# Optimization experiments

Hardware: AMD Instinct MI355X
Metric: run time of the kernel (lower is better)

The kernel has to match this reference:

```python
import jax, jax.numpy as jnp
import numpy as np

N, K = 150000, 27
C1, C2 = 64, 64
CLAMP = 1.0


def _lrelu(v):
    return jnp.where(v >= 0, v, 0.2 * v)


def _sparse_conv(feats, nbr_idx, W):
    # feats: [N, Cin], nbr_idx: [N, K], W: [K, Cin, Cout]
    # gather-GEMM-scatter sparse conv; scan over the 27 fixed kernel offsets
    acc0 = jnp.zeros((feats.shape[0], W.shape[-1]), feats.dtype)

    def step(acc, kw):
        idx, Wk = kw  # idx: [N], Wk: [Cin, Cout]
        return acc + feats[idx] @ Wk, None

    acc, _ = jax.lax.scan(step, acc0, (nbr_idx.T, W))
    return acc


def _bottleneck(x, nbr_idx, w1, w2, w3):
    h = _lrelu(_sparse_conv(x, nbr_idx, w1))  # kxkxk conv
    h = _lrelu(h @ w2)                        # 1x1x1 conv
    return _sparse_conv(h, nbr_idx, w3)       # kxkxk conv


def setup_inputs() -> dict:
    key = jax.random.key(0)
    ks = jax.random.split(key, 14)
    x = jax.random.normal(ks[0], (N, C1 + C2), jnp.float32)
    nbr_idx = jax.random.randint(ks[1], (N, K), 0, N, jnp.int32)
    s = 0.1  # xavier-like small scale
    d = {"x": x, "nbr_idx": nbr_idx}
    names = ["g1", "g2", "h1", "h2"]
    for i, nm in enumerate(names):
        d[nm + "_w1"] = jax.random.normal(ks[2 + 3 * i], (K, C2 if nm in ("g2", "h2") else C1, C1 if nm in ("g2", "h2") else C2), jnp.float32) * s
        co = C1 if nm in ("g2", "h2") else C2
        d[nm + "_w2"] = jax.random.normal(ks[3 + 3 * i], (co, co), jnp.float32) * s
        d[nm + "_w3"] = jax.random.normal(ks[4 + 3 * i], (K, co, co), jnp.float32) * s
    return d


def reference(x, nbr_idx, g1_w1, g1_w2, g1_w3, g2_w1, g2_w2, g2_w3,
              h1_w1, h1_w2, h1_w3, h2_w1, h2_w2, h2_w3):
    x1 = x[:, :C1]
    x2 = x[:, C1:C1 + C2]
    # forward (reverse=False) affine coupling
    s1 = jnp.exp(CLAMP * (jax.nn.sigmoid(_bottleneck(x2, nbr_idx, g2_w1, g2_w2, g2_w3)) * 2 - 1))
    y1 = x1 * s1 + _bottleneck(x2, nbr_idx, h2_w1, h2_w2, h2_w3)
    s2 = jnp.exp(CLAMP * (jax.nn.sigmoid(_bottleneck(y1, nbr_idx, g1_w1, g1_w2, g1_w3)) * 2 - 1))
    y2 = x2 * s2 + _bottleneck(y1, nbr_idx, h1_w1, h1_w2, h1_w3)
    return jnp.concatenate([y1, y2], axis=1)
```

## Files before the change

### kernel.cpp

```cpp
#include <hip/hip_runtime.h>
#include <stdint.h>

typedef unsigned short u16;
typedef __bf16 bf16x8 __attribute__((ext_vector_type(8)));
typedef float f32x4 __attribute__((ext_vector_type(4)));

#define NNODES 150000
#define KNBR 27
#define LDX 128
#define MR 64
#define APAD 72
#define WSU 8192

#define WAITVM(N) asm volatile("s_waitcnt vmcnt(" #N ")" ::: "memory")

static __device__ __forceinline__ void gl_lds16(const u16* g, u16* l){
  __builtin_amdgcn_global_load_lds((const __attribute__((address_space(1))) void*)g,
                                   (__attribute__((address_space(3))) void*)l, 16, 0, 0);
}

static __device__ __forceinline__ u16 f2bf(float f){
  union { float f; uint32_t i; } v; v.f = f;
  uint32_t x = v.i;
  uint32_t r = (x + 0x7fffu + ((x >> 16) & 1u)) >> 16;
  return (u16)r;
}
static __device__ __forceinline__ float lrelu(float v){ return v >= 0.f ? v : 0.2f*v; }

__global__ void reformat_w(const float* __restrict__ src, u16* __restrict__ dst, int ksteps){
  int idx = blockIdx.x*256 + threadIdx.x;
  int total = ksteps*4*64;
  if (idx >= total) return;
  int lane = idx & 63;
  int ctile = (idx >> 6) & 3;
  int t = idx >> 8;
  int quad = lane >> 4, m = lane & 15;
  union { u16 h[8]; float4 v; } tmp;
  const float* s = src + ((size_t)(t*32 + quad*8))*64 + ctile*16 + m;
  #pragma unroll
  for (int j=0;j<8;j++) tmp.h[j] = f2bf(s[j*64]);
  *reinterpret_cast<float4*>(dst + (size_t)idx*8) = tmp.v;
}

__global__ void conv_x2(const float* __restrict__ x, u16* __restrict__ sb){
  int idx = blockIdx.x*256 + threadIdx.x;
  int e = idx*8;
  if (e >= NNODES*64) return;
  int row = e >> 6, col = e & 63;
  const float* s = x + (size_t)row*LDX + 64 + col;
  float4 a = *reinterpret_cast<const float4*>(s);
  float4 b = *reinterpret_cast<const float4*>(s+4);
  union { u16 h[8]; float4 v; } t;
  t.h[0]=f2bf(a.x); t.h[1]=f2bf(a.y); t.h[2]=f2bf(a.z); t.h[3]=f2bf(a.w);
  t.h[4]=f2bf(b.x); t.h[5]=f2bf(b.y); t.h[6]=f2bf(b.z); t.h[7]=f2bf(b.w);
  *reinterpret_cast<float4*>(sb + e) = t.v;
}

__global__ __launch_bounds__(256,4) void conv1_fused(
    const u16* __restrict__ sb,
    const int* __restrict__ nbr,
    const u16* __restrict__ wb1g, const u16* __restrict__ wb1h,
    const u16* __restrict__ wb2g, const u16* __restrict__ wb2h,
    u16* __restrict__ u)
{
  extern __shared__ char smem[];
  u16* ws    = (u16*)smem;
  int* s_idx = (int*)(smem + 2*WSU*2);
  u16* sa    = (u16*)smem;

  int tid = threadIdx.x;
  int row0 = blockIdx.x * MR;
  for (int i = tid; i < MR*KNBR; i += 256){
    int r = i / KNBR, kk = i - r*KNBR;
    int row = row0 + r;
    s_idx[i] = (row < NNODES) ? nbr[row*KNBR + kk] : 0;
  }
  __syncthreads();

  int lane = tid & 63;
  int wv = tid >> 6;
  int quad = lane >> 4, m = lane & 15;
  int qoff = quad * 8;
  int tt_w = wv >> 1, mat_w = wv & 1;
  const u16* wsrc = mat_w ? wb1h : wb1g;
  const int* idx = &s_idx[(wv*16 + m)*KNBR];

  f32x4 acc[2][4];
  f32x4 zz = {0.f,0.f,0.f,0.f};
  #pragma unroll
  for (int mt2=0;mt2<2;mt2++)
    #pragma unroll
    for (int i=0;i<4;i++) acc[mt2][i] = zz;

  bf16x8 as[3][2];

  #define STAGE_W1(s) { \
    u16* dst_ = ws + ((s)&1)*WSU + (tt_w*2+mat_w)*2048; \
    const u16* src_ = wsrc + ((size_t)(2*(s)+tt_w))*2048 + (size_t)lane*8; \
    _Pragma("unroll") \
    for (int ct_=0; ct_<4; ct_++) gl_lds16(src_ + ct_*512, dst_ + ct_*512); }

  #define LOAD_A1(s, d0, d1) { \
    const u16* r_ = sb + (size_t)idx[s]*64 + qoff; \
    d0 = *reinterpret_cast<const bf16x8*>(r_); \
    d1 = *reinterpret_cast<const bf16x8*>(r_ + 32); }

  STAGE_W1(0); __builtin_amdgcn_sched_barrier(0);
  LOAD_A1(0, as[0][0], as[0][1]); __builtin_amdgcn_sched_barrier(0);
  LOAD_A1(1, as[1][0], as[1][1]); __builtin_amdgcn_sched_barrier(0);
  LOAD_A1(2, as[2][0], as[2][1]);

  #pragma unroll
  for (int k=0;k<KNBR;k++){
    if (k == 0)       { WAITVM(4); }
    else if (k <= 24) { WAITVM(2); }
    else              { WAITVM(0); }
    __builtin_amdgcn_s_barrier();

    if (k+1 < KNBR) { STAGE_W1(k+1); }
    __builtin_amdgcn_sched_barrier(0);

    const u16* wsb = ws + (k&1)*WSU;
    #pragma unroll
    for (int tt=0;tt<2;tt++){
      bf16x8 af = as[k%3][tt];
      #pragma unroll
      for (int mt2=0;mt2<2;mt2++){
        #pragma unroll
        for (int ct=0;ct<4;ct++){
          bf16x8 b = *reinterpret_cast<const bf16x8*>(wsb + ((tt*2+mt2)*4+ct)*512 + (size_t)lane*8);
          acc[mt2][ct] = __builtin_amdgcn_mfma_f32_16x16x32_bf16(af, b, acc[mt2][ct], 0,0,0);
        }
      }
    }
    if (k+3 < KNBR) { LOAD_A1(k+3, as[k%3][0], as[k%3][1]); }
  }
  __syncthreads();

  #pragma unroll
  for (int mt2=0;mt2<2;mt2++){
    #pragma unroll
    for (int ct=0;ct<4;ct++){
      #pragma unroll
      for (int i=0;i<4;i++){
        int rl = wv*16 + quad*4 + i;
        sa[mt2*MR*APAD + rl*APAD + ct*16 + m] = f2bf(lrelu(acc[mt2][ct][i]));
      }
    }
  }
  f32x4 d[2][4];
  #pragma unroll
  for (int mt2=0;mt2<2;mt2++)
    #pragma unroll
    for (int i=0;i<4;i++) d[mt2][i] = zz;
  #pragma unroll
  for (int c=0;c<2;c++){
    #pragma unroll
    for (int mt2=0;mt2<2;mt2++){
      bf16x8 a = *reinterpret_cast<const bf16x8*>(&sa[mt2*MR*APAD + (wv*16 + m)*APAD + c*32 + qoff]);
      #pragma unroll
      for (int ct=0;ct<4;ct++){
        const u16* wp = (mt2 ? wb2h : wb2g) + (((size_t)c*4+ct)*64 + lane)*8;
        bf16x8 b = *reinterpret_cast<const bf16x8*>(wp);
        d[mt2][ct] = __builtin_amdgcn_mfma_f32_16x16x32_bf16(a, b, d[mt2][ct], 0,0,0);
      }
    }
  }
  #pragma unroll
  for (int mt2=0;mt2<2;mt2++){
    #pragma unroll
    for (int ct=0;ct<4;ct++){
      #pragma unroll
      for (int i=0;i<4;i++){
        int row = row0 + wv*16 + quad*4 + i;
        if (row < NNODES){
          u[(size_t)row*128 + mt2*64 + ct*16 + m] = f2bf(lrelu(d[mt2][ct][i]));
        }
      }
    }
  }
  #undef STAGE_W1
  #undef LOAD_A1
}

__global__ __launch_bounds__(256,4) void conv2_coupling(
    const u16* __restrict__ ub,
    const int* __restrict__ nbr,
    const u16* __restrict__ wbg, const u16* __restrict__ wbh,
    const float* __restrict__ x, int xcol0,
    float* __restrict__ out, int ycol0,
    u16* __restrict__ yb, int write_yb)
{
  extern __shared__ char smem[];
  u16* ws    = (u16*)smem;
  int* s_idx = (int*)(smem + 2*WSU*2);

  int tid = threadIdx.x;
  int row0 = blockIdx.x * MR;
  for (int i = tid; i < MR*KNBR; i += 256){
    int r = i / KNBR, kk = i - r*KNBR;
    int row = row0 + r;
    s_idx[i] = (row < NNODES) ? nbr[row*KNBR + kk] : 0;
  }
  __syncthreads();

  int lane = tid & 63;
  int wv = tid >> 6;
  int quad = lane >> 4, m = lane & 15;
  int qoff = quad * 8;
  int tt_w = wv >> 1, mat_w = wv & 1;
  const u16* wsrc = mat_w ? wbh : wbg;
  const int* idx = &s_idx[(wv*16 + m)*KNBR];

  f32x4 accg[4], acch[4];
  f32x4 zz = {0.f,0.f,0.f,0.f};
  #pragma unroll
  for (int i=0;i<4;i++){ accg[i]=zz; acch[i]=zz; }

  bf16x8 as[2][4];

  #define STAGE_W2(s) { \
    u16* dst_ = ws + ((s)&1)*WSU + (tt_w*2+mat_w)*2048; \
    const u16* src_ = wsrc + ((size_t)(2*(s)+tt_w))*2048 + (size_t)lane*8; \
    _Pragma("unroll") \
    for (int ct_=0; ct_<4; ct_++) gl_lds16(src_ + ct_*512, dst_ + ct_*512); }

  #define LOAD_A2(s, d0, d1, d2, d3) { \
    const u16* r_ = ub + (size_t)idx[s]*128 + qoff; \
    d0 = *reinterpret_cast<const bf16x8*>(r_); \
    d1 = *reinterpret_cast<const bf16x8*>(r_ + 32); \
    d2 = *reinterpret_cast<const bf16x8*>(r_ + 64); \
    d3 = *reinterpret_cast<const bf16x8*>(r_ + 96); }

  STAGE_W2(0); __builtin_amdgcn_sched_barrier(0);
  LOAD_A2(0, as[0][0], as[0][1], as[0][2], as[0][3]); __builtin_amdgcn_sched_barrier(0);
  LOAD_A2(1, as[1][0], as[1][1], as[1][2], as[1][3]);

  #pragma unroll
  for (int k=0;k<KNBR;k++){
    if (k <= 25) { WAITVM(4); }
    else         { WAITVM(0); }
    __builtin_amdgcn_s_barrier();

    if (k+1 < KNBR) { STAGE_W2(k+1); }
    __builtin_amdgcn_sched_barrier(0);

    const u16* wsb = ws + (k&1)*WSU;
    #pragma unroll
    for (int tt=0;tt<2;tt++){
      bf16x8 ag = as[k&1][tt];
      bf16x8 ah = as[k&1][2+tt];
      #pragma unroll
      for (int ct=0;ct<4;ct++){
        bf16x8 bg = *reinterpret_cast<const bf16x8*>(wsb + ((tt*2+0)*4+ct)*512 + (size_t)lane*8);
        accg[ct] = __builtin_amdgcn_mfma_f32_16x16x32_bf16(ag, bg, accg[ct], 0,0,0);
      }
      #pragma unroll
      for (int ct=0;ct<4;ct++){
        bf16x8 bh = *reinterpret_cast<const bf16x8*>(wsb + ((tt*2+1)*4+ct)*512 + (size_t)lane*8);
        acch[ct] = __builtin_amdgcn_mfma_f32_16x16x32_bf16(ah, bh, acch[ct], 0,0,0);
      }
    }
    if (k+2 < KNBR) { LOAD_A2(k+2, as[k&1][0], as[k&1][1], as[k&1][2], as[k&1][3]); }
  }

  #pragma unroll
  for (int ct=0;ct<4;ct++){
    #pragma unroll
    for (int i=0;i<4;i++){
      int row = row0 + wv*16 + quad*4 + i;
      if (row < NNODES){
        int col = ct*16 + m;
        float bg = accg[ct][i];
        float bh = acch[ct][i];
        float s = 1.f/(1.f + __expf(-bg));
        s = __expf(2.f*s - 1.f);
        float xv = x[(size_t)row*LDX + xcol0 + col];
        float y = xv*s + bh;
        out[(size_t)row*LDX + ycol0 + col] = y;
        if (write_yb) yb[(size_t)row*64 + col] = f2bf(y);
      }
    }
  }
  #undef STAGE_W2
  #undef LOAD_A2
}

extern "C" void kernel_launch(void* const* d_in, const int* in_sizes, int n_in,
                              void* d_out, int out_size, void* d_ws, size_t ws_size,
                              hipStream_t stream)
{
  const float* x   = (const float*)d_in[0];
  const int*   nbr = (const int*)d_in[1];
  const float* g1_w1=(const float*)d_in[2],  *g1_w2=(const float*)d_in[3],  *g1_w3=(const float*)d_in[4];
  const float* g2_w1=(const float*)d_in[5],  *g2_w2=(const float*)d_in[6],  *g2_w3=(const float*)d_in[7];
  const float* h1_w1=(const float*)d_in[8],  *h1_w2=(const float*)d_in[9],  *h1_w3=(const float*)d_in[10];
  const float* h2_w1=(const float*)d_in[11], *h2_w2=(const float*)d_in[12], *h2_w3=(const float*)d_in[13];
  float* out = (float*)d_out;
  u16* ws = (u16*)d_ws;

  const size_t WBB = (size_t)54*4*64*8;
  const size_t WBS = (size_t)2*4*64*8;
  u16* p = ws;
  u16* wb_g2_1=p; p+=WBB;  u16* wb_h2_1=p; p+=WBB;
  u16* wb_g2_2=p; p+=WBS;  u16* wb_h2_2=p; p+=WBS;
  u16* wb_g2_3=p; p+=WBB;  u16* wb_h2_3=p; p+=WBB;
  u16* wb_g1_1=p; p+=WBB;  u16* wb_h1_1=p; p+=WBB;
  u16* wb_g1_2=p; p+=WBS;  u16* wb_h1_2=p; p+=WBS;
  u16* wb_g1_3=p; p+=WBB;  u16* wb_h1_3=p; p+=WBB;
  u16* ub = p; p += (size_t)NNODES*128;
  u16* sb = p; p += (size_t)NNODES*64;

  reformat_w<<<54,256,0,stream>>>(g2_w1, wb_g2_1, 54);
  reformat_w<<<54,256,0,stream>>>(h2_w1, wb_h2_1, 54);
  reformat_w<<<2,256,0,stream>>>(g2_w2, wb_g2_2, 2);
  reformat_w<<<2,256,0,stream>>>(h2_w2, wb_h2_2, 2);
  reformat_w<<<54,256,0,stream>>>(g2_w3, wb_g2_3, 54);
  reformat_w<<<54,256,0,stream>>>(h2_w3, wb_h2_3, 54);
  reformat_w<<<54,256,0,stream>>>(g1_w1, wb_g1_1, 54);
  reformat_w<<<54,256,0,stream>>>(h1_w1, wb_h1_1, 54);
  reformat_w<<<2,256,0,stream>>>(g1_w2, wb_g1_2, 2);
  reformat_w<<<2,256,0,stream>>>(h1_w2, wb_h1_2, 2);
  reformat_w<<<54,256,0,stream>>>(g1_w3, wb_g1_3, 54);
  reformat_w<<<54,256,0,stream>>>(h1_w3, wb_h1_3, 54);

  conv_x2<<<(NNODES*64/8 + 255)/256, 256, 0, stream>>>(x, sb);

  int nblk = (NNODES + MR - 1)/MR;
  size_t lds_sz = (size_t)2*WSU*2 + (size_t)MR*KNBR*4;

  conv1_fused<<<nblk,256,lds_sz,stream>>>(sb, nbr, wb_g2_1, wb_h2_1, wb_g2_2, wb_h2_2, ub);
  conv2_coupling<<<nblk,256,lds_sz,stream>>>(ub, nbr, wb_g2_3, wb_h2_3, x, 0, out, 0, sb, 1);
  conv1_fused<<<nblk,256,lds_sz,stream>>>(sb, nbr, wb_g1_1, wb_h1_1, wb_g1_2, wb_h1_2, ub);
  conv2_coupling<<<nblk,256,lds_sz,stream>>>(ub, nbr, wb_g1_3, wb_h1_3, x, 64, out, 64, sb, 0);
}
```

Baseline: 789.4 us.

## Double block rows to 128 with 512 threads sharing each weight stage

Each block now covers 128 rows with 8 waves, so every double-buffered weight slice in LDS is reused by twice as many waves. The cooperative staging macro is rewritten so each wave copies two 512-element chunks. In conv1 the 1x1 weights are also staged into LDS instead of being read from global memory by every wave. The cost is more LDS per block and larger barrier groups, which may lower occupancy and make the per-step barriers more expensive.

Result: faster. 745.6 us (-5.5%).

```diff
diff --git a/kernel.cpp b/kernel.cpp
--- a/kernel.cpp
+++ b/kernel.cpp
@@ -8,7 +8,7 @@
 #define NNODES 150000
 #define KNBR 27
 #define LDX 128
-#define MR 64
+#define MR 128
 #define APAD 72
 #define WSU 8192
 
@@ -56,7 +56,17 @@
   *reinterpret_cast<float4*>(sb + e) = t.v;
 }
 
-__global__ __launch_bounds__(256,4) void conv1_fused(
+#define STAGE_W(s, wG, wH) { \
+  u16* db_ = ws + ((s)&1)*WSU; \
+  _Pragma("unroll") \
+  for (int j_=0;j_<2;j_++){ \
+    int c_ = wv*2 + j_; \
+    int mat_ = (c_>>2)&1; int tt_ = c_>>3; int ct_ = c_&3; \
+    const u16* src_ = (mat_ ? (wH) : (wG)) + ((size_t)(2*(s)+tt_))*2048 + (size_t)ct_*512 + (size_t)lane*8; \
+    gl_lds16(src_, db_ + (size_t)c_*512); \
+  } }
+
+__global__ __launch_bounds__(512,4) void conv1_fused(
     const u16* __restrict__ sb,
     const int* __restrict__ nbr,
     const u16* __restrict__ wb1g, const u16* __restrict__ wb1h,
@@ -67,10 +77,11 @@
   u16* ws    = (u16*)smem;
   int* s_idx = (int*)(smem + 2*WSU*2);
   u16* sa    = (u16*)smem;
+  u16* w2l   = (u16*)(smem + 36864);
 
   int tid = threadIdx.x;
   int row0 = blockIdx.x * MR;
-  for (int i = tid; i < MR*KNBR; i += 256){
+  for (int i = tid; i < MR*KNBR; i += 512){
     int r = i / KNBR, kk = i - r*KNBR;
     int row = row0 + r;
     s_idx[i] = (row < NNODES) ? nbr[row*KNBR + kk] : 0;
@@ -81,8 +92,6 @@
   int wv = tid >> 6;
   int quad = lane >> 4, m = lane & 15;
   int qoff = quad * 8;
-  int tt_w = wv >> 1, mat_w = wv & 1;
-  const u16* wsrc = mat_w ? wb1h : wb1g;
   const int* idx = &s_idx[(wv*16 + m)*KNBR];
 
   f32x4 acc[2][4];
@@ -93,19 +102,13 @@
     for (int i=0;i<4;i++) acc[mt2][i] = zz;
 
   bf16x8 as[3][2];
-
-  #define STAGE_W1(s) { \
-    u16* dst_ = ws + ((s)&1)*WSU + (tt_w*2+mat_w)*2048; \
-    const u16* src_ = wsrc + ((size_t)(2*(s)+tt_w))*2048 + (size_t)lane*8; \
-    _Pragma("unroll") \
-    for (int ct_=0; ct_<4; ct_++) gl_lds16(src_ + ct_*512, dst_ + ct_*512); }
 
   #define LOAD_A1(s, d0, d1) { \
     const u16* r_ = sb + (size_t)idx[s]*64 + qoff; \
     d0 = *reinterpret_cast<const bf16x8*>(r_); \
     d1 = *reinterpret_cast<const bf16x8*>(r_ + 32); }
 
-  STAGE_W1(0); __builtin_amdgcn_sched_barrier(0);
+  STAGE_W(0, wb1g, wb1h); __builtin_amdgcn_sched_barrier(0);
   LOAD_A1(0, as[0][0], as[0][1]); __builtin_amdgcn_sched_barrier(0);
   LOAD_A1(1, as[1][0], as[1][1]); __builtin_amdgcn_sched_barrier(0);
   LOAD_A1(2, as[2][0], as[2][1]);
@@ -117,7 +120,7 @@
     else              { WAITVM(0); }
     __builtin_amdgcn_s_barrier();
 
-    if (k+1 < KNBR) { STAGE_W1(k+1); }
+    if (k+1 < KNBR) { STAGE_W(k+1, wb1g, wb1h); }
     __builtin_amdgcn_sched_barrier(0);
 
     const u16* wsb = ws + (k&1)*WSU;
@@ -138,6 +141,14 @@
   __syncthreads();
 
   #pragma unroll
+  for (int j_=0;j_<2;j_++){
+    int cc = wv*2 + j_;
+    int mt2_ = cc>>3;
+    const u16* src_ = (mt2_ ? wb2h : wb2g) + (size_t)(cc&7)*512 + (size_t)lane*8;
+    gl_lds16(src_, w2l + (size_t)cc*512);
+  }
+
+  #pragma unroll
   for (int mt2=0;mt2<2;mt2++){
     #pragma unroll
     for (int ct=0;ct<4;ct++){
@@ -148,6 +159,9 @@
       }
     }
   }
+  WAITVM(0);
+  __syncthreads();
+
   f32x4 d[2][4];
   #pragma unroll
   for (int mt2=0;mt2<2;mt2++)
@@ -160,8 +174,7 @@
       bf16x8 a = *reinterpret_cast<const bf16x8*>(&sa[mt2*MR*APAD + (wv*16 + m)*APAD + c*32 + qoff]);
       #pragma unroll
       for (int ct=0;ct<4;ct++){
-        const u16* wp = (mt2 ? wb2h : wb2g) + (((size_t)c*4+ct)*64 + lane)*8;
-        bf16x8 b = *reinterpret_cast<const bf16x8*>(wp);
+        bf16x8 b = *reinterpret_cast<const bf16x8*>(w2l + (size_t)(mt2*8 + c*4 + ct)*512 + (size_t)lane*8);
         d[mt2][ct] = __builtin_amdgcn_mfma_f32_16x16x32_bf16(a, b, d[mt2][ct], 0,0,0);
       }
     }
@@ -179,11 +192,10 @@
       }
     }
   }
-  #undef STAGE_W1
   #undef LOAD_A1
 }
 
-__global__ __launch_bounds__(256,4) void conv2_coupling(
+__global__ __launch_bounds__(512,4) void conv2_coupling(
     const u16* __restrict__ ub,
     const int* __restrict__ nbr,
     const u16* __restrict__ wbg, const u16* __restrict__ wbh,
@@ -197,7 +209,7 @@
 
   int tid = threadIdx.x;
   int row0 = blockIdx.x * MR;
-  for (int i = tid; i < MR*KNBR; i += 256){
+  for (int i = tid; i < MR*KNBR; i += 512){
     int r = i / KNBR, kk = i - r*KNBR;
     int row = row0 + r;
     s_idx[i] = (row < NNODES) ? nbr[row*KNBR + kk] : 0;
@@ -208,8 +220,6 @@
   int wv = tid >> 6;
   int quad = lane >> 4, m = lane & 15;
   int qoff = quad * 8;
-  int tt_w = wv >> 1, mat_w = wv & 1;
-  const u16* wsrc = mat_w ? wbh : wbg;
   const int* idx = &s_idx[(wv*16 + m)*KNBR];
 
   f32x4 accg[4], acch[4];
@@ -218,12 +228,6 @@
   for (int i=0;i<4;i++){ accg[i]=zz; acch[i]=zz; }
 
   bf16x8 as[2][4];
-
-  #define STAGE_W2(s) { \
-    u16* dst_ = ws + ((s)&1)*WSU + (tt_w*2+mat_w)*2048; \
-    const u16* src_ = wsrc + ((size_t)(2*(s)+tt_w))*2048 + (size_t)lane*8; \
-    _Pragma("unroll") \
-    for (int ct_=0; ct_<4; ct_++) gl_lds16(src_ + ct_*512, dst_ + ct_*512); }
 
   #define LOAD_A2(s, d0, d1, d2, d3) { \
     const u16* r_ = ub + (size_t)idx[s]*128 + qoff; \
@@ -232,17 +236,17 @@
     d2 = *reinterpret_cast<const bf16x8*>(r_ + 64); \
     d3 = *reinterpret_cast<const bf16x8*>(r_ + 96); }
 
-  STAGE_W2(0); __builtin_amdgcn_sched_barrier(0);
+  STAGE_W(0, wbg, wbh); __builtin_amdgcn_sched_barrier(0);
   LOAD_A2(0, as[0][0], as[0][1], as[0][2], as[0][3]); __builtin_amdgcn_sched_barrier(0);
   LOAD_A2(1, as[1][0], as[1][1], as[1][2], as[1][3]);
 
   #pragma unroll
   for (int k=0;k<KNBR;k++){
-    if (k <= 25) { WAITVM(4); }
-    else         { WAITVM(0); }
+    if (k < 26) { WAITVM(4); }
+    else        { WAITVM(0); }
     __builtin_amdgcn_s_barrier();
 
-    if (k+1 < KNBR) { STAGE_W2(k+1); }
+    if (k+1 < KNBR) { STAGE_W(k+1, wbg, wbh); }
     __builtin_amdgcn_sched_barrier(0);
 
     const u16* wsb = ws + (k&1)*WSU;
@@ -282,7 +286,6 @@
       }
     }
   }
-  #undef STAGE_W2
   #undef LOAD_A2
 }
 
@@ -327,10 +330,11 @@
   conv_x2<<<(NNODES*64/8 + 255)/256, 256, 0, stream>>>(x, sb);
 
   int nblk = (NNODES + MR - 1)/MR;
-  size_t lds_sz = (size_t)2*WSU*2 + (size_t)MR*KNBR*4;
-
-  conv1_fused<<<nblk,256,lds_sz,stream>>>(sb, nbr, wb_g2_1, wb_h2_1, wb_g2_2, wb_h2_2, ub);
-  conv2_coupling<<<nblk,256,lds_sz,stream>>>(ub, nbr, wb_g2_3, wb_h2_3, x, 0, out, 0, sb, 1);
-  conv1_fused<<<nblk,256,lds_sz,stream>>>(sb, nbr, wb_g1_1, wb_h1_1, wb_g1_2, wb_h1_2, ub);
-  conv2_coupling<<<nblk,256,lds_sz,stream>>>(ub, nbr, wb_g1_3, wb_h1_3, x, 64, out, 64, sb, 0);
-}
+  size_t c1_lds = 53248;
+  size_t c2_lds = (size_t)2*WSU*2 + (size_t)MR*KNBR*4;
+
+  conv1_fused<<<nblk,512,c1_lds,stream>>>(sb, nbr, wb_g2_1, wb_h2_1, wb_g2_2, wb_h2_2, ub);
+  conv2_coupling<<<nblk,512,c2_lds,stream>>>(ub, nbr, wb_g2_3, wb_h2_3, x, 0, out, 0, sb, 1);
+  conv1_fused<<<nblk,512,c1_lds,stream>>>(sb, nbr, wb_g1_1, wb_h1_1, wb_g1_2, wb_h1_2, ub);
+  conv2_coupling<<<nblk,512,c2_lds,stream>>>(ub, nbr, wb_g1_3, wb_h1_3, x, 64, out, 64, sb, 0);
+}
```
